# Optimization experiments

Hardware: AMD Instinct MI355X
Metric: run time of the kernel (lower is better)

The kernel has to match this reference:

```python
import jax, jax.numpy as jnp
import numpy as np

B, S, D = 16, 2048, 768
NORM = 1.0 / float(np.sqrt(D))


def setup_inputs() -> dict:
    key = jax.random.key(0)
    k1, k2, k3, k4, k5 = jax.random.split(key, 5)
    b_in = jax.random.normal(k1, (B, S, D), dtype=jnp.float32)
    mask = jax.random.randint(k2, (B, S), 0, 2, dtype=jnp.int64)
    # row 0 must be unmasked: the module returns attention[:, 0, :], and a fully
    # masked query row softmaxes all -inf -> NaN (same quirk as the torch source).
    mask = mask.at[:, 0].set(1)
    Wq = jax.random.normal(k3, (D, D), dtype=jnp.float32) * 0.02
    Wk = jax.random.normal(k4, (D, D), dtype=jnp.float32) * 0.02
    Wv = jax.random.normal(k5, (D, D), dtype=jnp.float32) * 0.02
    return {"b_in": b_in, "mask": mask, "Wq": Wq, "Wk": Wk, "Wv": Wv}


def reference(b_in, mask, Wq, Wk, Wv):
    # nn.Linear(bias=False): y = x @ W.T  (W is [out, in])
    q = jnp.einsum("bsd,ed->bse", b_in, Wq)
    k = jnp.einsum("bsd,ed->bse", b_in, Wk)
    v = jnp.einsum("bsd,ed->bse", b_in, Wv)
    # full [B, S, S] score matrix, as in the original bmm
    scores = jnp.einsum("bqd,bkd->bqk", q, k) * NORM
    # mask.unsqueeze(2): [B, S, 1] broadcasts over the KEY axis -> masks whole query rows
    scores = jnp.where(mask[:, :, None] == 0, -jnp.inf, scores)
    attn = jax.nn.softmax(scores, axis=-1)
    out = jnp.einsum("bqk,bkd->bqd", attn, v)
    return out[:, 0, :]
```

## Files before the change

kernel.cpp:

```cpp
#include <hip/hip_runtime.h>
#include <math.h>

#define BB 16
#define SS 2048
#define DD 768

#define NORM_SCALE 0.036084391824351615f

#define ECH 24
#define EPC (DD / ECH)

#define RPC 16
#define NCH (SS / RPC)

__global__ void rowdot_kernel(const float* __restrict__ src, size_t src_stride,
                              const float* __restrict__ W,
                              float* __restrict__ dst, float scale,
                              float* __restrict__ zero_buf) {
    int wid  = blockIdx.x * 4 + (threadIdx.x >> 6);
    int lane = threadIdx.x & 63;
    int b = wid / DD;
    int e = wid % DD;
    const float4* xr = (const float4*)(src + (size_t)b * src_stride);
    const float4* wr = (const float4*)(W + (size_t)e * DD);
    float acc = 0.f;
#pragma unroll
    for (int k = 0; k < 3; ++k) {
        float4 xv = xr[lane + k * 64];
        float4 wv = wr[lane + k * 64];
        acc += xv.x * wv.x + xv.y * wv.y + xv.z * wv.z + xv.w * wv.w;
    }
#pragma unroll
    for (int off = 32; off > 0; off >>= 1) acc += __shfl_down(acc, off);
    if (lane == 0) dst[wid] = acc * scale;
    if (zero_buf != nullptr && lane == 1) zero_buf[wid] = 0.f;
}

__global__ void kq_split_kernel(const float* __restrict__ q0,
                                const float* __restrict__ Wk,
                                float* __restrict__ kqs) {
    __shared__ float qs[EPC];
    int echunk = blockIdx.x;
    int b      = blockIdx.y;
    int t      = threadIdx.x;
    if (t < EPC) qs[t] = q0[b * DD + echunk * EPC + t];
    __syncthreads();
    const float4* Wk4 = (const float4*)(Wk + (size_t)(echunk * EPC) * DD);
    float4 acc = {0.f, 0.f, 0.f, 0.f};
#pragma unroll 4
    for (int e = 0; e < EPC; ++e) {
        float q = qs[e];
        float4 w = Wk4[e * (DD / 4) + t];
        acc.x += q * w.x;
        acc.y += q * w.y;
        acc.z += q * w.z;
        acc.w += q * w.w;
    }
    float* dst = kqs + b * DD + t * 4;
    atomicAdd(dst + 0, acc.x);
    atomicAdd(dst + 1, acc.y);
    atomicAdd(dst + 2, acc.z);
    atomicAdd(dst + 3, acc.w);
}

__global__ void __launch_bounds__(256) flash_kernel(
        const float* __restrict__ x,
        const float* __restrict__ kqs,
        float* __restrict__ m_part,
        float* __restrict__ l_part,
        float* __restrict__ o_part) {
    __shared__ float4 osh[4 * 192];
    __shared__ float sc[RPC];
    __shared__ float wsum[4];
    int chunk = blockIdx.x;
    int b     = blockIdx.y;
    int tid   = threadIdx.x;
    int wave  = tid >> 6, lane = tid & 63;
    int s0    = chunk * RPC;

    const float4* xr = (const float4*)(x + ((size_t)b * SS + s0 + wave * 4) * DD);
    float4 xv[12];
#pragma unroll
    for (int j = 0; j < 4; ++j)
#pragma unroll
        for (int k = 0; k < 3; ++k)
            xv[j * 3 + k] = xr[j * (DD / 4) + k * 64 + lane];

    const float4* kr = (const float4*)(kqs + b * DD);
    float4 kf[3];
#pragma unroll
    for (int k = 0; k < 3; ++k) kf[k] = kr[k * 64 + lane];

#pragma unroll
    for (int j = 0; j < 4; ++j) {
        float acc = 0.f;
#pragma unroll
        for (int k = 0; k < 3; ++k) {
            float4 xx = xv[j * 3 + k];
            acc += xx.x * kf[k].x + xx.y * kf[k].y
                 + xx.z * kf[k].z + xx.w * kf[k].w;
        }
#pragma unroll
        for (int off = 32; off > 0; off >>= 1) acc += __shfl_down(acc, off);
        if (lane == 0) sc[wave * 4 + j] = acc;
    }
    __syncthreads();

    float m = sc[0];
#pragma unroll
    for (int r = 1; r < RPC; ++r) m = fmaxf(m, sc[r]);

    float pl = (lane < 4) ? expf(sc[wave * 4 + lane] - m) : 0.f;
    float p0 = __shfl(pl, 0), p1 = __shfl(pl, 1);
    float p2 = __shfl(pl, 2), p3 = __shfl(pl, 3);
    if (lane == 0) wsum[wave] = p0 + p1 + p2 + p3;

#pragma unroll
    for (int k = 0; k < 3; ++k) {
        float4 a;
        a.x = p0 * xv[k].x + p1 * xv[3 + k].x + p2 * xv[6 + k].x + p3 * xv[9 + k].x;
        a.y = p0 * xv[k].y + p1 * xv[3 + k].y + p2 * xv[6 + k].y + p3 * xv[9 + k].y;
        a.z = p0 * xv[k].z + p1 * xv[3 + k].z + p2 * xv[6 + k].z + p3 * xv[9 + k].z;
        a.w = p0 * xv[k].w + p1 * xv[3 + k].w + p2 * xv[6 + k].w + p3 * xv[9 + k].w;
        osh[wave * 192 + k * 64 + lane] = a;
    }
    __syncthreads();

    int pidx = b * NCH + chunk;
    if (tid < 192) {
        float4 s0v = osh[tid], s1 = osh[192 + tid];
        float4 s2 = osh[384 + tid], s3 = osh[576 + tid];
        float4 s;
        s.x = s0v.x + s1.x + s2.x + s3.x;
        s.y = s0v.y + s1.y + s2.y + s3.y;
        s.z = s0v.z + s1.z + s2.z + s3.z;
        s.w = s0v.w + s1.w + s2.w + s3.w;
        ((float4*)(o_part + (size_t)pidx * DD))[tid] = s;
    }
    if (tid == 0) {
        m_part[pidx] = m;
        l_part[pidx] = wsum[0] + wsum[1] + wsum[2] + wsum[3];
    }
}

__global__ void combine_kernel(const float* __restrict__ m_part,
                               const float* __restrict__ l_part,
                               const float* __restrict__ o_part,
                               float* __restrict__ c) {
    __shared__ float w[NCH];
    __shared__ float bc[2];
    int b   = blockIdx.x;
    int seg = blockIdx.y;
    int tid = threadIdx.x;

    if (tid < 64) {
        float m = fmaxf(m_part[b * NCH + tid], m_part[b * NCH + tid + 64]);
#pragma unroll
        for (int off = 32; off > 0; off >>= 1) m = fmaxf(m, __shfl_down(m, off));
        if (tid == 0) bc[0] = m;
    }
    __syncthreads();
    float M = bc[0];
    if (tid < NCH) w[tid] = expf(m_part[b * NCH + tid] - M);
    __syncthreads();
    if (tid < 64) {
        float s = w[tid] * l_part[b * NCH + tid]
                + w[tid + 64] * l_part[b * NCH + tid + 64];
#pragma unroll
        for (int off = 32; off > 0; off >>= 1) s += __shfl_down(s, off);
        if (tid == 0) bc[1] = 1.f / s;
    }
    __syncthreads();
    float inv = bc[1];

    int col = seg * 256 + tid;
    const float* op = o_part + (size_t)b * NCH * DD + col;
    float a = 0.f;
#pragma unroll 8
    for (int cc = 0; cc < NCH; ++cc) a += w[cc] * op[(size_t)cc * DD];
    c[b * DD + col] = a * inv;
}

extern "C" void kernel_launch(void* const* d_in, const int* in_sizes, int n_in,
                              void* d_out, int out_size, void* d_ws, size_t ws_size,
                              hipStream_t stream) {
    const float* b_in = (const float*)d_in[0];
    const float* Wq = (const float*)d_in[2];
    const float* Wk = (const float*)d_in[3];
    const float* Wv = (const float*)d_in[4];
    float* out = (float*)d_out;

    float* ws     = (float*)d_ws;
    float* q0     = ws;
    float* kqs    = q0 + BB * DD;
    float* m_part = kqs + BB * DD;
    float* l_part = m_part + BB * NCH;
    float* o_part = l_part + BB * NCH;
    float* c      = o_part + (size_t)BB * NCH * DD;

    rowdot_kernel<<<BB * DD / 4, 256, 0, stream>>>(b_in, (size_t)SS * DD, Wq,
                                                   q0, NORM_SCALE, kqs);
    kq_split_kernel<<<dim3(ECH, BB), 192, 0, stream>>>(q0, Wk, kqs);
    flash_kernel<<<dim3(NCH, BB), 256, 0, stream>>>(b_in, kqs,
                                                    m_part, l_part, o_part);
    combine_kernel<<<dim3(BB, 3), 256, 0, stream>>>(m_part, l_part, o_part, c);
    rowdot_kernel<<<BB * DD / 4, 256, 0, stream>>>(c, (size_t)DD, Wv, out,
                                                   1.f, nullptr);
}
```

Before: 183.3 us.

## Fuse q0 and Wk projection, fuse combine with Wv projection, drop atomics

Merges the Wq row-dot and the Wk split kernel into one kernel that computes q0 slices in shared memory and writes per-chunk partial kq vectors instead of atomically adding them. The flash kernel now sums 16 partials itself. The combine step is fused with the final Wv projection. Kernel launches drop from five to three, and the atomics and the zero-init are removed. In exchange, every flash block re-reads 16 partial vectors, and the combine blocks repeat the o_part reduction for each of the 8 e-segments.

```diff
diff --git a/kernel.cpp b/kernel.cpp
--- a/kernel.cpp
+++ b/kernel.cpp
@@ -7,65 +7,60 @@
 
 #define NORM_SCALE 0.036084391824351615f
 
-#define ECH 24
-#define EPC (DD / ECH)
+#define ECH2 16
+#define EPC2 (DD / ECH2)
 
 #define RPC 16
 #define NCH (SS / RPC)
 
-__global__ void rowdot_kernel(const float* __restrict__ src, size_t src_stride,
-                              const float* __restrict__ W,
-                              float* __restrict__ dst, float scale,
-                              float* __restrict__ zero_buf) {
-    int wid  = blockIdx.x * 4 + (threadIdx.x >> 6);
-    int lane = threadIdx.x & 63;
-    int b = wid / DD;
-    int e = wid % DD;
-    const float4* xr = (const float4*)(src + (size_t)b * src_stride);
-    const float4* wr = (const float4*)(W + (size_t)e * DD);
+#define ESEG 8
+#define EPB (DD / ESEG)
+
+__global__ void __launch_bounds__(192) qk_fused_kernel(
+        const float* __restrict__ x, const float* __restrict__ Wq,
+        const float* __restrict__ Wk, float* __restrict__ kq_part) {
+    __shared__ float4 xs4[192];
+    __shared__ float part[192];
+    __shared__ float q0s[EPC2];
+    int ec = blockIdx.x;
+    int b  = blockIdx.y;
+    int t  = threadIdx.x;
+    int e0 = ec * EPC2;
+
+    const float4* xr = (const float4*)(x + (size_t)b * SS * DD);
+    xs4[t] = xr[t];
+    __syncthreads();
+
+    int g = t >> 2, i = t & 3;
+    const float4* wq = (const float4*)(Wq + (size_t)(e0 + g) * DD);
     float acc = 0.f;
-#pragma unroll
-    for (int k = 0; k < 3; ++k) {
-        float4 xv = xr[lane + k * 64];
-        float4 wv = wr[lane + k * 64];
+#pragma unroll 8
+    for (int j = 0; j < 48; ++j) {
+        float4 xv = xs4[j * 4 + i];
+        float4 wv = wq[j * 4 + i];
         acc += xv.x * wv.x + xv.y * wv.y + xv.z * wv.z + xv.w * wv.w;
     }
-#pragma unroll
-    for (int off = 32; off > 0; off >>= 1) acc += __shfl_down(acc, off);
-    if (lane == 0) dst[wid] = acc * scale;
-    if (zero_buf != nullptr && lane == 1) zero_buf[wid] = 0.f;
-}
-
-__global__ void kq_split_kernel(const float* __restrict__ q0,
-                                const float* __restrict__ Wk,
-                                float* __restrict__ kqs) {
-    __shared__ float qs[EPC];
-    int echunk = blockIdx.x;
-    int b      = blockIdx.y;
-    int t      = threadIdx.x;
-    if (t < EPC) qs[t] = q0[b * DD + echunk * EPC + t];
-    __syncthreads();
-    const float4* Wk4 = (const float4*)(Wk + (size_t)(echunk * EPC) * DD);
-    float4 acc = {0.f, 0.f, 0.f, 0.f};
+    part[t] = acc;
+    __syncthreads();
+    if (t < EPC2)
+        q0s[t] = NORM_SCALE *
+                 (part[t * 4] + part[t * 4 + 1] + part[t * 4 + 2] + part[t * 4 + 3]);
+    __syncthreads();
+
+    const float4* wk = (const float4*)(Wk + (size_t)e0 * DD);
+    float4 a = {0.f, 0.f, 0.f, 0.f};
 #pragma unroll 4
-    for (int e = 0; e < EPC; ++e) {
-        float q = qs[e];
-        float4 w = Wk4[e * (DD / 4) + t];
-        acc.x += q * w.x;
-        acc.y += q * w.y;
-        acc.z += q * w.z;
-        acc.w += q * w.w;
-    }
-    float* dst = kqs + b * DD + t * 4;
-    atomicAdd(dst + 0, acc.x);
-    atomicAdd(dst + 1, acc.y);
-    atomicAdd(dst + 2, acc.z);
-    atomicAdd(dst + 3, acc.w);
+    for (int e = 0; e < EPC2; ++e) {
+        float q  = q0s[e];
+        float4 w = wk[e * 192 + t];
+        a.x += q * w.x; a.y += q * w.y; a.z += q * w.z; a.w += q * w.w;
+    }
+    ((float4*)(kq_part + ((size_t)b * ECH2 + ec) * DD))[t] = a;
 }
 
 __global__ void __launch_bounds__(256) flash_kernel(
         const float* __restrict__ x,
-        const float* __restrict__ kqs,
+        const float* __restrict__ kq_part,
         float* __restrict__ m_part,
         float* __restrict__ l_part,
         float* __restrict__ o_part) {
@@ -86,10 +81,17 @@
         for (int k = 0; k < 3; ++k)
             xv[j * 3 + k] = xr[j * (DD / 4) + k * 64 + lane];
 
-    const float4* kr = (const float4*)(kqs + b * DD);
+    const float4* kp = (const float4*)(kq_part + (size_t)b * ECH2 * DD);
     float4 kf[3];
-#pragma unroll
-    for (int k = 0; k < 3; ++k) kf[k] = kr[k * 64 + lane];
+    kf[0] = kf[1] = kf[2] = make_float4(0.f, 0.f, 0.f, 0.f);
+#pragma unroll 4
+    for (int ec = 0; ec < ECH2; ++ec) {
+#pragma unroll
+        for (int k = 0; k < 3; ++k) {
+            float4 tv = kp[ec * 192 + k * 64 + lane];
+            kf[k].x += tv.x; kf[k].y += tv.y; kf[k].z += tv.z; kf[k].w += tv.w;
+        }
+    }
 
 #pragma unroll
     for (int j = 0; j < 4; ++j) {
@@ -143,42 +145,61 @@
     }
 }
 
-__global__ void combine_kernel(const float* __restrict__ m_part,
-                               const float* __restrict__ l_part,
-                               const float* __restrict__ o_part,
-                               float* __restrict__ c) {
+__global__ void __launch_bounds__(192) combine_out_kernel(
+        const float* __restrict__ m_part, const float* __restrict__ l_part,
+        const float* __restrict__ o_part, const float* __restrict__ Wv,
+        float* __restrict__ out) {
     __shared__ float w[NCH];
+    __shared__ float4 c4s[192];
     __shared__ float bc[2];
-    int b   = blockIdx.x;
-    int seg = blockIdx.y;
-    int tid = threadIdx.x;
-
-    if (tid < 64) {
-        float m = fmaxf(m_part[b * NCH + tid], m_part[b * NCH + tid + 64]);
+    int b  = blockIdx.x;
+    int es = blockIdx.y;
+    int t  = threadIdx.x;
+
+    if (t < 64) {
+        float m = fmaxf(m_part[b * NCH + t], m_part[b * NCH + t + 64]);
 #pragma unroll
         for (int off = 32; off > 0; off >>= 1) m = fmaxf(m, __shfl_down(m, off));
-        if (tid == 0) bc[0] = m;
+        if (t == 0) bc[0] = m;
     }
     __syncthreads();
     float M = bc[0];
-    if (tid < NCH) w[tid] = expf(m_part[b * NCH + tid] - M);
-    __syncthreads();
-    if (tid < 64) {
-        float s = w[tid] * l_part[b * NCH + tid]
-                + w[tid + 64] * l_part[b * NCH + tid + 64];
+    if (t < NCH) w[t] = expf(m_part[b * NCH + t] - M);
+    __syncthreads();
+    if (t < 64) {
+        float s = w[t] * l_part[b * NCH + t]
+                + w[t + 64] * l_part[b * NCH + t + 64];
 #pragma unroll
         for (int off = 32; off > 0; off >>= 1) s += __shfl_down(s, off);
-        if (tid == 0) bc[1] = 1.f / s;
+        if (t == 0) bc[1] = 1.f / s;
     }
     __syncthreads();
     float inv = bc[1];
 
-    int col = seg * 256 + tid;
-    const float* op = o_part + (size_t)b * NCH * DD + col;
-    float a = 0.f;
+    const float4* op4 = (const float4*)(o_part + (size_t)b * NCH * DD);
+    float4 a = {0.f, 0.f, 0.f, 0.f};
+#pragma unroll 16
+    for (int cc = 0; cc < NCH; ++cc) {
+        float4 v = op4[(size_t)cc * 192 + t];
+        float ww = w[cc];
+        a.x += ww * v.x; a.y += ww * v.y; a.z += ww * v.z; a.w += ww * v.w;
+    }
+    a.x *= inv; a.y *= inv; a.z *= inv; a.w *= inv;
+    c4s[t] = a;
+    __syncthreads();
+
+    int r = t >> 1, i = t & 1;
+    int e = es * EPB + r;
+    const float4* wv = (const float4*)(Wv + (size_t)e * DD);
+    float acc = 0.f;
 #pragma unroll 8
-    for (int cc = 0; cc < NCH; ++cc) a += w[cc] * op[(size_t)cc * DD];
-    c[b * DD + col] = a * inv;
+    for (int j = 0; j < 96; ++j) {
+        float4 wvv = wv[j * 2 + i];
+        float4 cv  = c4s[j * 2 + i];
+        acc += cv.x * wvv.x + cv.y * wvv.y + cv.z * wvv.z + cv.w * wvv.w;
+    }
+    acc += __shfl_xor(acc, 1);
+    if (i == 0) out[b * DD + e] = acc;
 }
 
 extern "C" void kernel_launch(void* const* d_in, const int* in_sizes, int n_in,
@@ -190,20 +211,15 @@
     const float* Wv = (const float*)d_in[4];
     float* out = (float*)d_out;
 
-    float* ws     = (float*)d_ws;
-    float* q0     = ws;
-    float* kqs    = q0 + BB * DD;
-    float* m_part = kqs + BB * DD;
-    float* l_part = m_part + BB * NCH;
-    float* o_part = l_part + BB * NCH;
-    float* c      = o_part + (size_t)BB * NCH * DD;
-
-    rowdot_kernel<<<BB * DD / 4, 256, 0, stream>>>(b_in, (size_t)SS * DD, Wq,
-                                                   q0, NORM_SCALE, kqs);
-    kq_split_kernel<<<dim3(ECH, BB), 192, 0, stream>>>(q0, Wk, kqs);
-    flash_kernel<<<dim3(NCH, BB), 256, 0, stream>>>(b_in, kqs,
+    float* ws      = (float*)d_ws;
+    float* kq_part = ws;
+    float* m_part  = kq_part + (size_t)BB * ECH2 * DD;
+    float* l_part  = m_part + BB * NCH;
+    float* o_part  = l_part + BB * NCH;
+
+    qk_fused_kernel<<<dim3(ECH2, BB), 192, 0, stream>>>(b_in, Wq, Wk, kq_part);
+    flash_kernel<<<dim3(NCH, BB), 256, 0, stream>>>(b_in, kq_part,
                                                     m_part, l_part, o_part);
-    combine_kernel<<<dim3(BB, 3), 256, 0, stream>>>(m_part, l_part, o_part, c);
-    rowdot_kernel<<<BB * DD / 4, 256, 0, stream>>>(c, (size_t)DD, Wv, out,
-                                                   1.f, nullptr);
-}
+    combine_out_kernel<<<dim3(BB, ESEG), 192, 0, stream>>>(m_part, l_part,
+                                                           o_part, Wv, out);
+}
```

New measurement: 190.4 us. 3.8% more time.
